# Optimization experiments

Measured on AMD Instinct MI355X. Metric: run time of the kernel, lower is better.

## Reference

```python
import jax, jax.numpy as jnp
import numpy as np

H, M = 1024, 8
HM = H * M
DT, TM, TA, TZI, TZJ, TP = 0.001, 0.05, 2.7, 0.24, 0.24, 10.0
EPS = np.float32(np.finfo(np.float32).tiny)


def log_eps(x):
    return jnp.log(jnp.where(x <= 0.0, EPS, x))


def setup_inputs() -> dict:
    key = jax.random.key(0)
    ks = jax.random.split(key, 13)
    f32 = jnp.float32
    return {
        "x": jax.random.uniform(ks[0], (H, M), f32),
        "s": jax.random.normal(ks[1], (H, M), f32),
        "o": jax.random.uniform(ks[2], (H, M), f32),
        "a": jax.random.normal(ks[3], (H, M), f32) * 0.1,
        "zi": jax.random.uniform(ks[4], (H, M), f32),
        "zj": jax.random.uniform(ks[5], (H, M), f32),
        "p": jax.random.uniform(ks[6], (), f32),
        "pi": jax.random.uniform(ks[7], (H, M), f32),
        "pj": jax.random.uniform(ks[8], (H, M), f32),
        "pij": jax.random.uniform(ks[9], (HM, HM), f32),
        "b": jax.random.normal(ks[10], (H, M), f32),
        "w": jax.random.normal(ks[11], (HM, HM), f32) * 0.01,
        "noise": jax.random.normal(ks[12], (H, M), f32),
        "ga": jnp.float32(1.0),
        "gw": jnp.float32(1.0),
        "gb": jnp.float32(1.0),
        "gs": jnp.float32(0.1),
        "k": jnp.float32(1.0),
    }


def reference(x, s, o, a, zi, zj, p, pi, pj, pij, b, w, noise, ga, gw, gb, gs, k):
    # --- update_state (train=True uses gw) ---
    st = gw * (b.reshape(-1) + w.T @ o.reshape(-1))          # GEMV, [HM]
    s_new = s + DT / TM * (st.reshape(H, M) - a + log_eps(x) + gs * noise - s)
    o_new = jax.nn.softmax(s_new, axis=1)
    a_new = a + DT / TA * (ga * o_new - a)
    # --- update_traces ---
    zi_new = zi + DT / TZI * (o_new - zi)
    zj_new = zj + DT / TZJ * (o_new - zj)
    # --- update_probabilities ---
    c = k * DT / TP
    p_new = p + c * (1.0 - p)
    pi_new = pi + c * (zi_new - pi)
    pj_new = pj + c * (zj_new - pj)
    pij_new = pij + c * (jnp.outer(zi_new.reshape(-1), zj_new.reshape(-1)) - pij)
    # --- update_connections ---
    w_new = log_eps(p_new * pij_new / jnp.outer(pi_new.reshape(-1), pj_new.reshape(-1)))
    b_new = gb * log_eps(pj_new)
    # torch forward returns o (buffers updated in place); JAX returns full new state
    return (o_new, s_new, a_new, zi_new, zj_new, p_new, pi_new, pj_new, pij_new, w_new, b_new)
```

## Files before the change

### kernel.cpp

```cpp
#include <hip/hip_runtime.h>
#include <math.h>

#define H_N 1024
#define M_N 8
#define HM 8192
#define NIC 64

typedef float f32x4 __attribute__((ext_vector_type(4)));
typedef float f32x4u __attribute__((ext_vector_type(4), aligned(4)));

static __device__ __forceinline__ float log_eps(float x) {
    const float EPS_TINY = 1.17549435e-38f;
    return __logf(x <= 0.0f ? EPS_TINY : x);
}

__global__ __launch_bounds__(256) void gemv_partial(const float* __restrict__ w,
                                                    const float* __restrict__ o,
                                                    float* __restrict__ pbuf) {
    const int jb = blockIdx.x & 7;
    const int ic = blockIdx.x >> 3;
    const int j0 = jb * 1024 + threadIdx.x * 4;
    const int i0 = ic * 128;
    f32x4 acc = {0.f, 0.f, 0.f, 0.f};
    const float* wp = w + (size_t)i0 * HM + j0;
#pragma unroll 4
    for (int i = 0; i < 128; ++i) {
        const float ov = o[i0 + i];
        const f32x4 wv = *reinterpret_cast<const f32x4*>(wp);
        acc.x += wv.x * ov; acc.y += wv.y * ov; acc.z += wv.z * ov; acc.w += wv.w * ov;
        wp += HM;
    }
    *reinterpret_cast<f32x4*>(&pbuf[(size_t)ic * HM + j0]) = acc;
}

__global__ __launch_bounds__(256) void row_kernel(
    const float* __restrict__ x, const float* __restrict__ s,
    const float* __restrict__ a, const float* __restrict__ zi,
    const float* __restrict__ zj, const float* __restrict__ p,
    const float* __restrict__ pi, const float* __restrict__ pj,
    const float* __restrict__ b, const float* __restrict__ noise,
    const float* __restrict__ ga, const float* __restrict__ gw,
    const float* __restrict__ gb, const float* __restrict__ gs,
    const float* __restrict__ k, const float* __restrict__ pbuf,
    float* __restrict__ out) {
    const int r = blockIdx.x * blockDim.x + threadIdx.x;
    if (r >= H_N) return;

    const float gwv = gw[0], gav = ga[0], gbv = gb[0], gsv = gs[0], kv = k[0], pv = p[0];
    const float c = kv * 1e-4f;

    float* o_new  = out;
    float* s_new  = out + (size_t)HM;
    float* a_new  = out + (size_t)2 * HM;
    float* zi_new = out + (size_t)3 * HM;
    float* zj_new = out + (size_t)4 * HM;
    float* p_new  = out + (size_t)5 * HM;
    float* pi_new = out + (size_t)5 * HM + 1;
    float* pj_new = out + (size_t)6 * HM + 1;
    float* b_new  = out + (size_t)7 * HM + 1 + (size_t)2 * HM * HM;

    const int base = r * M_N;

    f32x4 r0 = {0.f, 0.f, 0.f, 0.f}, r1 = {0.f, 0.f, 0.f, 0.f};
#pragma unroll 8
    for (int ic = 0; ic < NIC; ++ic) {
        const float* pp = pbuf + (size_t)ic * HM + base;
        const f32x4 v0 = *reinterpret_cast<const f32x4*>(pp);
        const f32x4 v1 = *reinterpret_cast<const f32x4*>(pp + 4);
        r0.x += v0.x; r0.y += v0.y; r0.z += v0.z; r0.w += v0.w;
        r1.x += v1.x; r1.y += v1.y; r1.z += v1.z; r1.w += v1.w;
    }
    const float stv[M_N] = {r0.x, r0.y, r0.z, r0.w, r1.x, r1.y, r1.z, r1.w};

    float sv[M_N], ev[M_N];
    float mx = -3.0e38f;
#pragma unroll
    for (int m = 0; m < M_N; ++m) {
        const int i = base + m;
        const float st = gwv * (b[i] + stv[m]);
        const float sn = s[i] + 0.02f * (st - a[i] + log_eps(x[i]) + gsv * noise[i] - s[i]);
        sv[m] = sn;
        mx = fmaxf(mx, sn);
    }
    float sum = 0.f;
#pragma unroll
    for (int m = 0; m < M_N; ++m) { ev[m] = __expf(sv[m] - mx); sum += ev[m]; }
    const float rs = 1.0f / sum;
#pragma unroll
    for (int m = 0; m < M_N; ++m) {
        const int i = base + m;
        const float on  = ev[m] * rs;
        const float an  = a[i]  + (float)(0.001 / 2.7)  * (gav * on - a[i]);
        const float zin = zi[i] + (float)(0.001 / 0.24) * (on - zi[i]);
        const float zjn = zj[i] + (float)(0.001 / 0.24) * (on - zj[i]);
        const float pin = pi[i] + c * (zin - pi[i]);
        const float pjn = pj[i] + c * (zjn - pj[i]);
        o_new[i]  = on;
        s_new[i]  = sv[m];
        a_new[i]  = an;
        zi_new[i] = zin;
        zj_new[i] = zjn;
        pi_new[i] = pin;
        pj_new[i] = pjn;
        b_new[i]  = gbv * log_eps(pjn);
    }
    if (r == 0) p_new[0] = pv + c * (1.0f - pv);
}

__global__ __launch_bounds__(256) void outer_kernel(
    const float* __restrict__ pij, const float* __restrict__ out_ro,
    float* __restrict__ out, const float* __restrict__ p,
    const float* __restrict__ k) {
    const float* zi_new = out_ro + (size_t)3 * HM;
    const float* zj_new = out_ro + (size_t)4 * HM;
    const float* pi_new = out_ro + (size_t)5 * HM + 1;
    const float* pj_new = out_ro + (size_t)6 * HM + 1;
    float* pij_new = out + (size_t)7 * HM + 1;
    float* w_new   = pij_new + (size_t)HM * HM;

    const float kv = k[0], pv = p[0];
    const float c  = kv * 1e-4f;
    const float pn = pv + c * (1.0f - pv);

    const size_t nvec   = (size_t)HM * HM / 4;
    const size_t stride = (size_t)gridDim.x * blockDim.x;
    for (size_t v = (size_t)blockIdx.x * blockDim.x + threadIdx.x; v < nvec; v += stride) {
        const size_t idx = v * 4;
        const int I = (int)(idx >> 13);
        const int J = (int)(idx & 8191);
        const float ziI = zi_new[I];
        const float piI = pi_new[I];
        const f32x4 pv4 = *reinterpret_cast<const f32x4*>(&pij[idx]);
        const f32x4  zj4 = *reinterpret_cast<const f32x4*>(&zj_new[J]);
        const f32x4u pj4 = *reinterpret_cast<const f32x4u*>(&pj_new[J]);

        const float q0 = pv4.x + c * (ziI * zj4.x - pv4.x);
        const float q1 = pv4.y + c * (ziI * zj4.y - pv4.y);
        const float q2 = pv4.z + c * (ziI * zj4.z - pv4.z);
        const float q3 = pv4.w + c * (ziI * zj4.w - pv4.w);

        __builtin_nontemporal_store(q0, &pij_new[idx + 0]);
        __builtin_nontemporal_store(q1, &pij_new[idx + 1]);
        __builtin_nontemporal_store(q2, &pij_new[idx + 2]);
        __builtin_nontemporal_store(q3, &pij_new[idx + 3]);

        const float v0 = __fdividef(pn * q0, piI * pj4.x);
        const float v1 = __fdividef(pn * q1, piI * pj4.y);
        const float v2 = __fdividef(pn * q2, piI * pj4.z);
        const float v3 = __fdividef(pn * q3, piI * pj4.w);

        __builtin_nontemporal_store(log_eps(v0), &w_new[idx + 0]);
        __builtin_nontemporal_store(log_eps(v1), &w_new[idx + 1]);
        __builtin_nontemporal_store(log_eps(v2), &w_new[idx + 2]);
        __builtin_nontemporal_store(log_eps(v3), &w_new[idx + 3]);
    }
}

extern "C" void kernel_launch(void* const* d_in, const int* in_sizes, int n_in,
                              void* d_out, int out_size, void* d_ws, size_t ws_size,
                              hipStream_t stream) {
    const float* x     = (const float*)d_in[0];
    const float* s     = (const float*)d_in[1];
    const float* o     = (const float*)d_in[2];
    const float* a     = (const float*)d_in[3];
    const float* zi    = (const float*)d_in[4];
    const float* zj    = (const float*)d_in[5];
    const float* p     = (const float*)d_in[6];
    const float* pi    = (const float*)d_in[7];
    const float* pj    = (const float*)d_in[8];
    const float* pij   = (const float*)d_in[9];
    const float* b     = (const float*)d_in[10];
    const float* w     = (const float*)d_in[11];
    const float* noise = (const float*)d_in[12];
    const float* ga    = (const float*)d_in[13];
    const float* gw    = (const float*)d_in[14];
    const float* gb    = (const float*)d_in[15];
    const float* gs    = (const float*)d_in[16];
    const float* k     = (const float*)d_in[17];

    float* out  = (float*)d_out;
    float* pbuf = (float*)d_ws;

    gemv_partial<<<512, 256, 0, stream>>>(w, o, pbuf);
    row_kernel<<<(H_N + 255) / 256, 256, 0, stream>>>(
        x, s, a, zi, zj, p, pi, pj, b, noise, ga, gw, gb, gs, k, pbuf, out);
    outer_kernel<<<2048, 256, 0, stream>>>(pij, out, out, p, k);
}
```

Baseline: 260.8 us.

## Split outer update into separate pij and w kernels

Splits the fused outer-product kernel into two launches: the first writes pij_new, the second reads pij_new back from memory to compute w_new. The scalar nontemporal stores become regular vector stores (unaligned-typed f32x4). This adds a full extra read of the 256MB pij_new array and one more kernel launch, which is extra memory traffic on a bandwidth-bound step. It likely trades that for simpler store patterns per kernel.

```diff
diff --git a/kernel.cpp b/kernel.cpp
--- a/kernel.cpp
+++ b/kernel.cpp
@@ -107,52 +107,60 @@
     if (r == 0) p_new[0] = pv + c * (1.0f - pv);
 }
 
-__global__ __launch_bounds__(256) void outer_kernel(
+__global__ __launch_bounds__(256) void outer_a(
     const float* __restrict__ pij, const float* __restrict__ out_ro,
-    float* __restrict__ out, const float* __restrict__ p,
-    const float* __restrict__ k) {
+    float* __restrict__ out, const float* __restrict__ k) {
     const float* zi_new = out_ro + (size_t)3 * HM;
     const float* zj_new = out_ro + (size_t)4 * HM;
-    const float* pi_new = out_ro + (size_t)5 * HM + 1;
-    const float* pj_new = out_ro + (size_t)6 * HM + 1;
     float* pij_new = out + (size_t)7 * HM + 1;
-    float* w_new   = pij_new + (size_t)HM * HM;
+
+    const float c = k[0] * 1e-4f;
+
+    const size_t nvec = (size_t)HM * HM / 4;
+    const size_t S    = (size_t)gridDim.x * blockDim.x;
+    for (size_t v = (size_t)blockIdx.x * blockDim.x + threadIdx.x; v < nvec; v += S) {
+        const size_t idx = v * 4;
+        const int I = (int)(idx >> 13);
+        const int J = (int)(idx & 8191);
+        const float ziI = zi_new[I];
+        const f32x4 pv4 = *reinterpret_cast<const f32x4*>(&pij[idx]);
+        const f32x4 zj4 = *reinterpret_cast<const f32x4*>(&zj_new[J]);
+        f32x4 Q;
+        Q.x = pv4.x + c * (ziI * zj4.x - pv4.x);
+        Q.y = pv4.y + c * (ziI * zj4.y - pv4.y);
+        Q.z = pv4.z + c * (ziI * zj4.z - pv4.z);
+        Q.w = pv4.w + c * (ziI * zj4.w - pv4.w);
+        *reinterpret_cast<f32x4u*>(&pij_new[idx]) = Q;
+    }
+}
+
+__global__ __launch_bounds__(256) void outer_b(
+    const float* __restrict__ out_ro, float* __restrict__ out,
+    const float* __restrict__ p, const float* __restrict__ k) {
+    const float* pi_new  = out_ro + (size_t)5 * HM + 1;
+    const float* pj_new  = out_ro + (size_t)6 * HM + 1;
+    const float* pij_new = out_ro + (size_t)7 * HM + 1;
+    float* w_new = out + (size_t)7 * HM + 1 + (size_t)HM * HM;
 
     const float kv = k[0], pv = p[0];
     const float c  = kv * 1e-4f;
     const float pn = pv + c * (1.0f - pv);
 
-    const size_t nvec   = (size_t)HM * HM / 4;
-    const size_t stride = (size_t)gridDim.x * blockDim.x;
-    for (size_t v = (size_t)blockIdx.x * blockDim.x + threadIdx.x; v < nvec; v += stride) {
+    const size_t nvec = (size_t)HM * HM / 4;
+    const size_t S    = (size_t)gridDim.x * blockDim.x;
+    for (size_t v = (size_t)blockIdx.x * blockDim.x + threadIdx.x; v < nvec; v += S) {
         const size_t idx = v * 4;
         const int I = (int)(idx >> 13);
         const int J = (int)(idx & 8191);
-        const float ziI = zi_new[I];
         const float piI = pi_new[I];
-        const f32x4 pv4 = *reinterpret_cast<const f32x4*>(&pij[idx]);
-        const f32x4  zj4 = *reinterpret_cast<const f32x4*>(&zj_new[J]);
+        const f32x4u q4  = *reinterpret_cast<const f32x4u*>(&pij_new[idx]);
         const f32x4u pj4 = *reinterpret_cast<const f32x4u*>(&pj_new[J]);
-
-        const float q0 = pv4.x + c * (ziI * zj4.x - pv4.x);
-        const float q1 = pv4.y + c * (ziI * zj4.y - pv4.y);
-        const float q2 = pv4.z + c * (ziI * zj4.z - pv4.z);
-        const float q3 = pv4.w + c * (ziI * zj4.w - pv4.w);
-
-        __builtin_nontemporal_store(q0, &pij_new[idx + 0]);
-        __builtin_nontemporal_store(q1, &pij_new[idx + 1]);
-        __builtin_nontemporal_store(q2, &pij_new[idx + 2]);
-        __builtin_nontemporal_store(q3, &pij_new[idx + 3]);
-
-        const float v0 = __fdividef(pn * q0, piI * pj4.x);
-        const float v1 = __fdividef(pn * q1, piI * pj4.y);
-        const float v2 = __fdividef(pn * q2, piI * pj4.z);
-        const float v3 = __fdividef(pn * q3, piI * pj4.w);
-
-        __builtin_nontemporal_store(log_eps(v0), &w_new[idx + 0]);
-        __builtin_nontemporal_store(log_eps(v1), &w_new[idx + 1]);
-        __builtin_nontemporal_store(log_eps(v2), &w_new[idx + 2]);
-        __builtin_nontemporal_store(log_eps(v3), &w_new[idx + 3]);
+        f32x4 W;
+        W.x = log_eps(__fdividef(pn * q4.x, piI * pj4.x));
+        W.y = log_eps(__fdividef(pn * q4.y, piI * pj4.y));
+        W.z = log_eps(__fdividef(pn * q4.z, piI * pj4.z));
+        W.w = log_eps(__fdividef(pn * q4.w, piI * pj4.w));
+        *reinterpret_cast<f32x4u*>(&w_new[idx]) = W;
     }
 }
 
@@ -184,5 +192,6 @@
     gemv_partial<<<512, 256, 0, stream>>>(w, o, pbuf);
     row_kernel<<<(H_N + 255) / 256, 256, 0, stream>>>(
         x, s, a, zi, zj, p, pi, pj, b, noise, ga, gw, gb, gs, k, pbuf, out);
-    outer_kernel<<<2048, 256, 0, stream>>>(pij, out, out, p, k);
+    outer_a<<<2048, 256, 0, stream>>>(pij, out, out, k);
+    outer_b<<<2048, 256, 0, stream>>>(out, out, p, k);
 }
```

New measurement: 295.7 us. +13.3%, slower.
